# Optimization experiments

Measured on AMD Instinct MI355X. Metric: run time of the kernel, lower is better.

The kernel has to match this reference:

```python
import jax, jax.numpy as jnp
import numpy as np

EMBED_DIM = 2048
NUM_HEADS = 16
HEAD_DIM = EMBED_DIM // NUM_HEADS
BATCH, SEQ = 4, 4096


def setup_inputs() -> dict:
    key = jax.random.key(0)
    k1, k2, k3, k4 = jax.random.split(key, 4)
    scale = 1.0 / np.sqrt(EMBED_DIM)
    x = jax.random.normal(k1, (BATCH, SEQ, EMBED_DIM), dtype=jnp.float32)
    W_qkv = jax.random.normal(k2, (EMBED_DIM, 3 * EMBED_DIM), dtype=jnp.float32) * scale
    W_out = jax.random.normal(k3, (EMBED_DIM, EMBED_DIM), dtype=jnp.float32) * scale
    b_out = jax.random.normal(k4, (EMBED_DIM,), dtype=jnp.float32) * 0.01
    return {"x": x, "W_qkv": W_qkv, "W_out": W_out, "b_out": b_out}


def reference(x, W_qkv, W_out, b_out):
    b, s, _ = x.shape
    # qkv: (b, s, 3, h, d)
    qkv = (x @ W_qkv).reshape(b, s, 3, NUM_HEADS, HEAD_DIM)
    q, k, v = qkv[:, :, 0], qkv[:, :, 1], qkv[:, :, 2]
    # NOTE: faithful to source — scores mix HEADS per token: (b, s, h, h)
    scores = jnp.einsum('bshd,bsHd->bshH', q, k) / jnp.sqrt(jnp.float32(HEAD_DIM))
    w = jax.nn.softmax(scores, axis=-1)
    attn = jnp.einsum('bshH,bsHd->bshd', w, v).reshape(b, s, EMBED_DIM)
    return attn @ W_out + b_out
```

## Files before the change

kernel.cpp:

```cpp
#include <hip/hip_runtime.h>
#include <hip/hip_bf16.h>
#include <cstdint>


#define TOKENS 16384
#define EMB    2048
#define NQKV   6144

typedef __bf16 bf16x8_t __attribute__((ext_vector_type(8)));
typedef float  f32x4_t  __attribute__((ext_vector_type(4)));

#define GLOAD16(gsrc, ldst)                                                    \
  __builtin_amdgcn_global_load_lds(                                            \
      (const __attribute__((address_space(1))) void*)(uintptr_t)(gsrc),        \
      (__attribute__((address_space(3))) void*)(uint32_t)(uintptr_t)(ldst),    \
      16, 0, 0)

static __device__ __forceinline__ unsigned short f32_to_bf16_bits(float f) {
  union { float f; uint32_t u; } x; x.f = f;
  uint32_t u = x.u;
  u += 0x7fffu + ((u >> 16) & 1u);
  return (unsigned short)(u >> 16);
}

__global__ __launch_bounds__(256) void cvt_f32_bf16(
    const float4* __restrict__ in, ushort4* __restrict__ out, int n4) {
  const int stride = gridDim.x * blockDim.x;
  for (int i = blockIdx.x * blockDim.x + threadIdx.x; i < n4; i += stride) {
    float4 v = in[i];
    ushort4 o;
    o.x = f32_to_bf16_bits(v.x);
    o.y = f32_to_bf16_bits(v.y);
    o.z = f32_to_bf16_bits(v.z);
    o.w = f32_to_bf16_bits(v.w);
    out[i] = o;
  }
}

__global__ __launch_bounds__(256) void transpose_cvt(
    const float* __restrict__ in, unsigned short* __restrict__ out, int R, int C) {
  __shared__ float tile[32][33];
  const int bx = blockIdx.x * 32;
  const int by = blockIdx.y * 32;
  const int tx = threadIdx.x;
  const int ty = threadIdx.y;
#pragma unroll
  for (int j = 0; j < 32; j += 8)
    tile[ty + j][tx] = in[(size_t)(by + ty + j) * C + bx + tx];
  __syncthreads();
#pragma unroll
  for (int j = 0; j < 32; j += 8)
    out[(size_t)(bx + ty + j) * R + by + tx] = f32_to_bf16_bits(tile[tx][ty + j]);
}

template <bool OUT_BF16>
__global__ __launch_bounds__(512, 1) void gemm_bt(
    const unsigned short* __restrict__ A,
    const unsigned short* __restrict__ BT,
    unsigned short* __restrict__ Cb,
    float* __restrict__ Cf,
    const float* __restrict__ bias,
    int M, int N) {
  constexpr int K = 2048;
  constexpr int BK = 64;
  constexpr int NKT = K / BK;
  __shared__ __align__(16) char lds[131072];

  const int nbx = N / 256;
  const int nwg = gridDim.x;
  const int bid = blockIdx.x;
  const int swzb = (bid & 7) * (nwg >> 3) + (bid >> 3);
  const int by = swzb / nbx;
  const int bx = swzb % nbx;

  const int t    = threadIdx.x;
  const int lane = t & 63;
  const int wid  = t >> 6;
  const int wr   = wid >> 2;
  const int wc   = wid & 3;
  const int lr   = lane & 15;
  const int g    = lane >> 4;

  const unsigned short* aSrc = A  + (size_t)by * 256 * K;
  const unsigned short* bSrc = BT + (size_t)bx * 256 * K;

  int aoff[2], boff[2];
#pragma unroll
  for (int i = 0; i < 2; ++i) {
    const int p   = (i * 512 + t) * 16;
    const int lo  = p ^ (((p >> 7) & 7) << 4);
    const int rih = lo >> 7;
    const int kbe = (lo & 127) >> 1;
    aoff[i] = (((rih >> 6) << 7) + (rih & 63)) * K + kbe;
    boff[i] = (((rih >> 5) << 6) + (rih & 31)) * K + kbe;
  }
  const int ldst = wid << 10;

  auto stageA = [&](int h, int k0, char* bufA) {
#pragma unroll
    for (int i = 0; i < 2; ++i)
      GLOAD16(aSrc + aoff[i] + h * (64 * K) + k0, bufA + h * 16384 + i * 8192 + ldst);
  };
  auto stageB = [&](int h, int k0, char* bufB) {
#pragma unroll
    for (int i = 0; i < 2; ++i)
      GLOAD16(bSrc + boff[i] + h * (32 * K) + k0, bufB + h * 16384 + i * 8192 + ldst);
  };

  const int sw   = (lr & 7) << 4;
  const int col0 = (g * 16) ^ sw;
  const int col1 = (64 + g * 16) ^ sw;
  const int aRow = (wr * 64 + lr) * 128;
  const int bRow = (wc * 32 + lr) * 128;

  f32x4_t acc[8][4] = {};
  bf16x8_t av0[4][2], av1[4][2];
  bf16x8_t bv0[2][2], bv1[2][2];

#define LDA_INTO(dst, bufA_, q)                                                \
  {                                                                            \
    const char* _b = (bufA_) + (q) * 16384 + aRow;                             \
    _Pragma("unroll") for (int m2 = 0; m2 < 4; ++m2) {                         \
      dst[m2][0] = *(const bf16x8_t*)(_b + m2 * 2048 + col0);                  \
      dst[m2][1] = *(const bf16x8_t*)(_b + m2 * 2048 + col1);                  \
    }                                                                          \
  }
#define LDB_INTO(dst, bufB_, pair)                                             \
  {                                                                            \
    _Pragma("unroll") for (int e = 0; e < 2; ++e) {                            \
      const int nf = (pair) * 2 + e;                                           \
      const char* _b = (bufB_) + (nf >> 1) * 16384 + (nf & 1) * 2048 + bRow;   \
      dst[e][0] = *(const bf16x8_t*)(_b + col0);                               \
      dst[e][1] = *(const bf16x8_t*)(_b + col1);                               \
    }                                                                          \
  }
#define MFMAQ(AV, BV, Q, PAIR)                                                 \
  _Pragma("unroll") for (int m2 = 0; m2 < 4; ++m2)                             \
  _Pragma("unroll") for (int e = 0; e < 2; ++e)                                \
  _Pragma("unroll") for (int ks = 0; ks < 2; ++ks)                             \
    acc[(Q) * 4 + m2][(PAIR) * 2 + e] = __builtin_amdgcn_mfma_f32_16x16x32_bf16( \
        AV[m2][ks], BV[e][ks], acc[(Q) * 4 + m2][(PAIR) * 2 + e], 0, 0, 0);

#define SBR __builtin_amdgcn_sched_barrier(0)
#define TAIL(N)                                                                \
  SBR; __builtin_amdgcn_s_barrier();                                           \
  asm volatile("s_waitcnt lgkmcnt(" #N ")" ::: "memory");                      \
  SBR; __builtin_amdgcn_s_setprio(1);
#define PEND                                                                   \
  __builtin_amdgcn_s_setprio(0); SBR; __builtin_amdgcn_s_barrier();

  {
    char* b0A = lds;
    char* b0B = lds + 32768;
    char* b1A = lds + 65536;
    char* b1B = b1A + 32768;
    stageA(0, 0, b0A); stageA(1, 0, b0A);
    stageB(0, 0, b0B); stageB(1, 0, b0B);
    stageA(0, BK, b1A);
    stageB(1, BK, b1B);
    asm volatile("s_waitcnt vmcnt(4)" ::: "memory");
    __builtin_amdgcn_s_barrier();
    LDA_INTO(av0, b0A, 0);
  }

  for (int kt = 0; kt < NKT; ++kt) {
    char* cA = lds + (kt & 1) * 65536;
    char* cB = cA + 32768;
    char* nA = lds + ((kt + 1) & 1) * 65536;
    char* nB = nA + 32768;
    const int k1 = (kt + 1) * BK;
    const int k2 = (kt + 2) * BK;
    const bool s1 = kt + 1 < NKT;
    const bool s2 = kt + 2 < NKT;

    LDB_INTO(bv0, cB, 0);
    if (s1) stageA(1, k1, nA);
    TAIL(0); MFMAQ(av0, bv0, 0, 0); PEND;

    LDB_INTO(bv1, cB, 1);
    LDA_INTO(av1, cA, 1);
    if (s1) stageB(0, k1, nB);
    TAIL(8); MFMAQ(av0, bv1, 0, 1); PEND;

    if (s2) stageA(0, k2, cA);
    TAIL(0); MFMAQ(av1, bv1, 1, 1); PEND;

    if (s2) stageB(1, k2, cB);
    if (s2) { asm volatile("s_waitcnt vmcnt(4)" ::: "memory"); }
    else    { asm volatile("s_waitcnt vmcnt(0)" ::: "memory"); }
    if (s1) {
      LDA_INTO(av0, nA, 0);
      TAIL(8);
    } else {
      TAIL(0);
    }
    MFMAQ(av1, bv0, 1, 0); PEND;
  }

  const int rbase = by * 256 + wr * 128 + g * 4;
  const int cbase = bx * 256 + wc * 64 + lr;
#pragma unroll
  for (int m = 0; m < 8; ++m) {
#pragma unroll
    for (int nf = 0; nf < 4; ++nf) {
      const int col = cbase + nf * 16;
#pragma unroll
      for (int j = 0; j < 4; ++j) {
        const size_t off = (size_t)(rbase + (m >> 2) * 64 + (m & 3) * 16 + j) * N + col;
        if constexpr (OUT_BF16) {
          Cb[off] = f32_to_bf16_bits(acc[m][nf][j]);
        } else {
          Cf[off] = acc[m][nf][j] + bias[col];
        }
      }
    }
  }
#undef LDA_INTO
#undef LDB_INTO
#undef MFMAQ
#undef SBR
#undef TAIL
#undef PEND
}

__global__ __launch_bounds__(256) void attn_heads(
    const unsigned short* __restrict__ qkv,
    unsigned short* __restrict__ attn) {
  __shared__ __align__(16) unsigned short sQKV[NQKV];
  __shared__ float sW[16][16];

  const int t = threadIdx.x;
  const size_t qbase = (size_t)blockIdx.x * NQKV;

  const uint4* gp = (const uint4*)(qkv + qbase);
  uint4* l = (uint4*)sQKV;
#pragma unroll
  for (int i = 0; i < 3; ++i) {
    const int idx = i * 256 + t;
    int dst = idx;
    if (idx >= 256 && idx < 512) {
      const int r = (idx - 256) >> 4;
      const int c = idx & 15;
      dst = 256 + r * 16 + (c ^ (r & 7));
    }
    l[dst] = gp[idx];
  }
  __syncthreads();

  const int h = t >> 4;
  const int H = t & 15;
  const bf16x8_t* q8 = (const bf16x8_t*)sQKV + h * 16;
  const bf16x8_t* k8 = (const bf16x8_t*)sQKV + 256;
  float s = 0.f;
#pragma unroll
  for (int d8 = 0; d8 < 16; ++d8) {
    bf16x8_t qv = q8[d8];
    bf16x8_t kv = k8[H * 16 + (d8 ^ (H & 7))];
#pragma unroll
    for (int j = 0; j < 8; ++j)
      s = fmaf((float)qv[j], (float)kv[j], s);
  }
  s *= 0.08838834764831843f;

  float mx = s;
#pragma unroll
  for (int o = 8; o; o >>= 1) mx = fmaxf(mx, __shfl_xor(mx, o));
  const float e = __expf(s - mx);
  float sum = e;
#pragma unroll
  for (int o = 8; o; o >>= 1) sum += __shfl_xor(sum, o);
  sW[h][H] = e / sum;
  __syncthreads();

  const int d0c = t & 15;
  const bf16x8_t* v8 = (const bf16x8_t*)sQKV + 512;
  float accv[8] = {};
#pragma unroll
  for (int j = 0; j < 16; ++j) {
    const float w = sW[h][j];
    const bf16x8_t vv = v8[j * 16 + d0c];
#pragma unroll
    for (int jj = 0; jj < 8; ++jj)
      accv[jj] = fmaf(w, (float)vv[jj], accv[jj]);
  }
  bf16x8_t o;
#pragma unroll
  for (int jj = 0; jj < 8; ++jj) o[jj] = (__bf16)accv[jj];
  *(bf16x8_t*)(attn + (size_t)blockIdx.x * EMB + h * 128 + d0c * 8) = o;
}

extern "C" void kernel_launch(void* const* d_in, const int* in_sizes, int n_in,
                              void* d_out, int out_size, void* d_ws, size_t ws_size,
                              hipStream_t stream) {
  const float* x    = (const float*)d_in[0];
  const float* Wqkv = (const float*)d_in[1];
  const float* Wout = (const float*)d_in[2];
  const float* bout = (const float*)d_in[3];
  float* out = (float*)d_out;

  unsigned short* xb    = (unsigned short*)d_ws;
  unsigned short* wqkvT = xb    + (size_t)33554432;
  unsigned short* woutT = wqkvT + (size_t)12582912;
  unsigned short* qkv   = woutT + (size_t)4194304;
  unsigned short* attn  = qkv   + (size_t)100663296;

  cvt_f32_bf16<<<2048, 256, 0, stream>>>((const float4*)x, (ushort4*)xb, 33554432 / 4);
  transpose_cvt<<<dim3(6144 / 32, 2048 / 32), dim3(32, 8), 0, stream>>>(Wqkv, wqkvT, 2048, 6144);
  transpose_cvt<<<dim3(2048 / 32, 2048 / 32), dim3(32, 8), 0, stream>>>(Wout, woutT, 2048, 2048);
  gemm_bt<true><<<(16384 / 256) * (6144 / 256), 512, 0, stream>>>(
      xb, wqkvT, qkv, nullptr, nullptr, 16384, 6144);
  attn_heads<<<TOKENS, 256, 0, stream>>>(qkv, attn);
  gemm_bt<false><<<(16384 / 256) * (2048 / 256), 512, 0, stream>>>(
      attn, woutT, nullptr, out, bout, 16384, 2048);
}
```

Measured before the change: 637.8 us.

## Make GEMM persistent with cross-tile prefetch of next output tile

Converts both GEMM launches into persistent kernels with 256 workgroups, each processing several 256x256 output tiles in sequence. The K-loop's prefetch pipeline now runs across tile boundaries, so the next tile's first K-slices are loaded while the current tile finishes. This removes per-workgroup launch, ramp-up and drain bubbles and tail-wave imbalance. The cost is a fixed tile-to-workgroup mapping with no dynamic balancing, plus an epilogue store that is no longer overlapped with another workgroup's compute.

```diff
diff --git a/kernel.cpp b/kernel.cpp
--- a/kernel.cpp
+++ b/kernel.cpp
@@ -53,25 +53,21 @@
     out[(size_t)(bx + ty + j) * R + by + tx] = f32_to_bf16_bits(tile[tx][ty + j]);
 }
 
-template <bool OUT_BF16>
+template <bool OUT_BF16, int ROUNDS, int NBX>
 __global__ __launch_bounds__(512, 1) void gemm_bt(
     const unsigned short* __restrict__ A,
     const unsigned short* __restrict__ BT,
     unsigned short* __restrict__ Cb,
     float* __restrict__ Cf,
-    const float* __restrict__ bias,
-    int M, int N) {
+    const float* __restrict__ bias) {
   constexpr int K = 2048;
   constexpr int BK = 64;
   constexpr int NKT = K / BK;
+  constexpr int N = NBX * 256;
   __shared__ __align__(16) char lds[131072];
 
-  const int nbx = N / 256;
-  const int nwg = gridDim.x;
   const int bid = blockIdx.x;
-  const int swzb = (bid & 7) * (nwg >> 3) + (bid >> 3);
-  const int by = swzb / nbx;
-  const int bx = swzb % nbx;
+  const int chunk = (bid & 7) * (32 * ROUNDS) + (bid >> 3);
 
   const int t    = threadIdx.x;
   const int lane = t & 63;
@@ -81,9 +77,6 @@
   const int lr   = lane & 15;
   const int g    = lane >> 4;
 
-  const unsigned short* aSrc = A  + (size_t)by * 256 * K;
-  const unsigned short* bSrc = BT + (size_t)bx * 256 * K;
-
   int aoff[2], boff[2];
 #pragma unroll
   for (int i = 0; i < 2; ++i) {
@@ -96,15 +89,15 @@
   }
   const int ldst = wid << 10;
 
-  auto stageA = [&](int h, int k0, char* bufA) {
+  auto stageA = [&](const unsigned short* src, int h, int k0, char* bufA) {
 #pragma unroll
     for (int i = 0; i < 2; ++i)
-      GLOAD16(aSrc + aoff[i] + h * (64 * K) + k0, bufA + h * 16384 + i * 8192 + ldst);
+      GLOAD16(src + aoff[i] + h * (64 * K) + k0, bufA + h * 16384 + i * 8192 + ldst);
   };
-  auto stageB = [&](int h, int k0, char* bufB) {
+  auto stageB = [&](const unsigned short* src, int h, int k0, char* bufB) {
 #pragma unroll
     for (int i = 0; i < 2; ++i)
-      GLOAD16(bSrc + boff[i] + h * (32 * K) + k0, bufB + h * 16384 + i * 8192 + ldst);
+      GLOAD16(src + boff[i] + h * (32 * K) + k0, bufB + h * 16384 + i * 8192 + ldst);
   };
 
   const int sw   = (lr & 7) << 4;
@@ -142,78 +135,102 @@
         AV[m2][ks], BV[e][ks], acc[(Q) * 4 + m2][(PAIR) * 2 + e], 0, 0, 0);
 
 #define SBR __builtin_amdgcn_sched_barrier(0)
-#define TAIL(N)                                                                \
+#define TAIL(NN)                                                               \
   SBR; __builtin_amdgcn_s_barrier();                                           \
-  asm volatile("s_waitcnt lgkmcnt(" #N ")" ::: "memory");                      \
+  asm volatile("s_waitcnt lgkmcnt(" #NN ")" ::: "memory");                     \
   SBR; __builtin_amdgcn_s_setprio(1);
 #define PEND                                                                   \
   __builtin_amdgcn_s_setprio(0); SBR; __builtin_amdgcn_s_barrier();
 
+  int tid = chunk;
+  int by = tid / NBX;
+  int bx = tid % NBX;
+  const unsigned short* aC = A  + (size_t)by * 256 * K;
+  const unsigned short* bC = BT + (size_t)bx * 256 * K;
   {
     char* b0A = lds;
     char* b0B = lds + 32768;
     char* b1A = lds + 65536;
     char* b1B = b1A + 32768;
-    stageA(0, 0, b0A); stageA(1, 0, b0A);
-    stageB(0, 0, b0B); stageB(1, 0, b0B);
-    stageA(0, BK, b1A);
-    stageB(1, BK, b1B);
+    stageA(aC, 0, 0, b0A); stageA(aC, 1, 0, b0A);
+    stageB(bC, 0, 0, b0B); stageB(bC, 1, 0, b0B);
+    stageA(aC, 0, BK, b1A);
+    stageB(bC, 1, BK, b1B);
     asm volatile("s_waitcnt vmcnt(4)" ::: "memory");
     __builtin_amdgcn_s_barrier();
     LDA_INTO(av0, b0A, 0);
   }
 
-  for (int kt = 0; kt < NKT; ++kt) {
-    char* cA = lds + (kt & 1) * 65536;
-    char* cB = cA + 32768;
-    char* nA = lds + ((kt + 1) & 1) * 65536;
-    char* nB = nA + 32768;
-    const int k1 = (kt + 1) * BK;
-    const int k2 = (kt + 2) * BK;
-    const bool s1 = kt + 1 < NKT;
-    const bool s2 = kt + 2 < NKT;
-
-    LDB_INTO(bv0, cB, 0);
-    if (s1) stageA(1, k1, nA);
-    TAIL(0); MFMAQ(av0, bv0, 0, 0); PEND;
-
-    LDB_INTO(bv1, cB, 1);
-    LDA_INTO(av1, cA, 1);
-    if (s1) stageB(0, k1, nB);
-    TAIL(8); MFMAQ(av0, bv1, 0, 1); PEND;
-
-    if (s2) stageA(0, k2, cA);
-    TAIL(0); MFMAQ(av1, bv1, 1, 1); PEND;
-
-    if (s2) stageB(1, k2, cB);
-    if (s2) { asm volatile("s_waitcnt vmcnt(4)" ::: "memory"); }
-    else    { asm volatile("s_waitcnt vmcnt(0)" ::: "memory"); }
-    if (s1) {
-      LDA_INTO(av0, nA, 0);
-      TAIL(8);
-    } else {
-      TAIL(0);
+  for (int r = 0; r < ROUNDS; ++r) {
+    const bool lastR = (r == ROUNDS - 1);
+    const int tidn = chunk + 32 * (lastR ? r : r + 1);
+    const int byn = tidn / NBX;
+    const int bxn = tidn % NBX;
+    const unsigned short* aN = A  + (size_t)byn * 256 * K;
+    const unsigned short* bN = BT + (size_t)bxn * 256 * K;
+
+    for (int kt = 0; kt < NKT; ++kt) {
+      char* cA = lds + (kt & 1) * 65536;
+      char* cB = cA + 32768;
+      char* nA = lds + ((kt + 1) & 1) * 65536;
+      char* nB = nA + 32768;
+      const bool w1 = (kt + 1 >= NKT);
+      const bool w2 = (kt + 2 >= NKT);
+      const bool s1 = !w1 || !lastR;
+      const bool s2 = !w2 || !lastR;
+      const unsigned short* A1 = w1 ? aN : aC;
+      const unsigned short* B1 = w1 ? bN : bC;
+      const unsigned short* A2 = w2 ? aN : aC;
+      const unsigned short* B2 = w2 ? bN : bC;
+      const int k1 = w1 ? 0 : (kt + 1) * BK;
+      const int k2 = w2 ? (kt + 2 - NKT) * BK : (kt + 2) * BK;
+
+      LDB_INTO(bv0, cB, 0);
+      if (s1) stageA(A1, 1, k1, nA);
+      TAIL(0); MFMAQ(av0, bv0, 0, 0); PEND;
+
+      LDB_INTO(bv1, cB, 1);
+      LDA_INTO(av1, cA, 1);
+      if (s1) stageB(B1, 0, k1, nB);
+      TAIL(8); MFMAQ(av0, bv1, 0, 1); PEND;
+
+      if (s2) stageA(A2, 0, k2, cA);
+      TAIL(0); MFMAQ(av1, bv1, 1, 1); PEND;
+
+      if (s2) stageB(B2, 1, k2, cB);
+      if (s2) { asm volatile("s_waitcnt vmcnt(4)" ::: "memory"); }
+      else    { asm volatile("s_waitcnt vmcnt(0)" ::: "memory"); }
+      if (s1) {
+        LDA_INTO(av0, nA, 0);
+        TAIL(8);
+      } else {
+        TAIL(0);
+      }
+      MFMAQ(av1, bv0, 1, 0); PEND;
     }
-    MFMAQ(av1, bv0, 1, 0); PEND;
-  }
-
-  const int rbase = by * 256 + wr * 128 + g * 4;
-  const int cbase = bx * 256 + wc * 64 + lr;
-#pragma unroll
-  for (int m = 0; m < 8; ++m) {
-#pragma unroll
-    for (int nf = 0; nf < 4; ++nf) {
-      const int col = cbase + nf * 16;
-#pragma unroll
-      for (int j = 0; j < 4; ++j) {
-        const size_t off = (size_t)(rbase + (m >> 2) * 64 + (m & 3) * 16 + j) * N + col;
-        if constexpr (OUT_BF16) {
-          Cb[off] = f32_to_bf16_bits(acc[m][nf][j]);
-        } else {
-          Cf[off] = acc[m][nf][j] + bias[col];
+
+    {
+      const int rbase = by * 256 + wr * 128 + g * 4;
+      const int cbase = bx * 256 + wc * 64 + lr;
+#pragma unroll
+      for (int m = 0; m < 8; ++m) {
+#pragma unroll
+        for (int nf = 0; nf < 4; ++nf) {
+          const int col = cbase + nf * 16;
+#pragma unroll
+          for (int j = 0; j < 4; ++j) {
+            const size_t off = (size_t)(rbase + (m >> 2) * 64 + (m & 3) * 16 + j) * N + col;
+            if constexpr (OUT_BF16) {
+              Cb[off] = f32_to_bf16_bits(acc[m][nf][j]);
+            } else {
+              Cf[off] = acc[m][nf][j] + bias[col];
+            }
+            acc[m][nf][j] = 0.0f;
+          }
         }
       }
     }
+    by = byn; bx = bxn; aC = aN; bC = bN;
   }
 #undef LDA_INTO
 #undef LDB_INTO
@@ -307,9 +324,9 @@
   cvt_f32_bf16<<<2048, 256, 0, stream>>>((const float4*)x, (ushort4*)xb, 33554432 / 4);
   transpose_cvt<<<dim3(6144 / 32, 2048 / 32), dim3(32, 8), 0, stream>>>(Wqkv, wqkvT, 2048, 6144);
   transpose_cvt<<<dim3(2048 / 32, 2048 / 32), dim3(32, 8), 0, stream>>>(Wout, woutT, 2048, 2048);
-  gemm_bt<true><<<(16384 / 256) * (6144 / 256), 512, 0, stream>>>(
-      xb, wqkvT, qkv, nullptr, nullptr, 16384, 6144);
+  gemm_bt<true, 6, 24><<<256, 512, 0, stream>>>(
+      xb, wqkvT, qkv, nullptr, nullptr);
   attn_heads<<<TOKENS, 256, 0, stream>>>(qkv, attn);
-  gemm_bt<false><<<(16384 / 256) * (2048 / 256), 512, 0, stream>>>(
-      attn, woutT, nullptr, out, bout, 16384, 2048);
-}
+  gemm_bt<false, 2, 8><<<256, 512, 0, stream>>>(
+      attn, woutT, nullptr, out, bout);
+}
```

Result: slower. 670.4 us (+5.1%).
